# Optimization experiments

Measured on AMD Instinct MI355X. Metric: run time of the kernel, lower is better.

## Reference

```python
import jax, jax.numpy as jnp
import numpy as np

NUM_EMBED = 1024
HEAD_SIZE = 64
B, T = 4, 4096

def setup_inputs() -> dict:
    key = jax.random.key(0)
    kx, kq, kk, kv = jax.random.split(key, 4)
    scale = NUM_EMBED ** -0.5
    return {
        "x": jax.random.normal(kx, (B, T, NUM_EMBED), dtype=jnp.float32),
        "Wq": jax.random.normal(kq, (NUM_EMBED, HEAD_SIZE), dtype=jnp.float32) * scale,
        "Wk": jax.random.normal(kk, (NUM_EMBED, HEAD_SIZE), dtype=jnp.float32) * scale,
        "Wv": jax.random.normal(kv, (NUM_EMBED, HEAD_SIZE), dtype=jnp.float32) * scale,
    }

def reference(x, Wq, Wk, Wv):
    # x: [B,T,C]; Wq/Wk/Wv: [C,H]
    q = jnp.einsum('btc,ch->bth', x, Wq)
    k = jnp.einsum('btc,ch->bth', x, Wk)
    v = jnp.einsum('btc,ch->bth', x, Wv)
    Tq = x.shape[1]
    att = jnp.einsum('bth,bsh->bts', q, k) * (k.shape[-1] ** -0.5)  # [B,T,T]
    causal = jnp.tril(jnp.ones((Tq, Tq), dtype=bool))
    att = jnp.where(causal, att, -jnp.inf)
    att = jax.nn.softmax(att, axis=-1)
    # dropout p=0 (eval mode): identity
    out = jnp.einsum('bts,bsh->bth', att, v)  # [B,T,H]
    return out
```

## Files before the change

### kernel.cpp

```cpp
#include <hip/hip_runtime.h>

#define B_ 4
#define T_ 4096
#define C_ 1024
#define H_ 64

typedef _Float16 half8  __attribute__((ext_vector_type(8)));
typedef _Float16 half4_ __attribute__((ext_vector_type(4)));
typedef float    floatx4 __attribute__((ext_vector_type(4)));

#define MFMA16(a, b, c)  __builtin_amdgcn_mfma_f32_16x16x32_f16(a, b, c, 0, 0, 0)
#define MFMA16K(a, b, c) __builtin_amdgcn_mfma_f32_16x16x16f16(a, b, c, 0, 0, 0)
#define LO4(v) __builtin_shufflevector(v, v, 0, 1, 2, 3)
#define HI4(v) __builtin_shufflevector(v, v, 4, 5, 6, 7)

__global__ __launch_bounds__(256) void pack_w_kn(
    const float* __restrict__ Wq, const float* __restrict__ Wk,
    const float* __restrict__ Wv, _Float16* __restrict__ Wt2)
{
    const int idx  = blockIdx.x * 256 + threadIdx.x;
    const int mt   = idx >> 14;
    const int j    = (idx >> 10) & 15;
    const int f    = (idx >> 9) & 1;
    const int lane = (idx >> 3) & 63;
    const int jj   = idx & 7;
    const int q = lane >> 4, c = lane & 15;
    const int k  = j * 64 + f * 32 + q * 8 + jj;
    const int hp = mt * 16 + c;
    const float* W = (hp < 64) ? Wq : (hp < 128) ? Wk : Wv;
    Wt2[idx] = (_Float16)W[k * H_ + (hp & 63)];
}

__global__ __launch_bounds__(512) void qkv_kn(
    const float* __restrict__ x, const _Float16* __restrict__ Wt2,
    _Float16* __restrict__ Qh, _Float16* __restrict__ Kpk,
    _Float16* __restrict__ Vpk)
{
    __shared__ _Float16 xs[2][32][72];
    const int tid  = threadIdx.x;
    const int lane = tid & 63, w = tid >> 6;
    const int q    = lane >> 4, c = lane & 15;
    const int nt   = w & 1;
    const int mg   = w >> 1;
    const int row0 = blockIdx.x * 32;

    const int srow = tid >> 4, scol = (tid & 15) * 4;
    const float* xg = x + (size_t)(row0 + srow) * C_ + scol;

    floatx4 acc[3];
    #pragma unroll
    for (int i = 0; i < 3; ++i) acc[i] = floatx4{0.f, 0.f, 0.f, 0.f};

    float4 g = *(const float4*)xg;

    for (int j = 0; j < 16; ++j) {
        half4_ hv;
        hv[0] = (_Float16)g.x; hv[1] = (_Float16)g.y;
        hv[2] = (_Float16)g.z; hv[3] = (_Float16)g.w;
        *(half4_*)(&xs[j & 1][srow][scol]) = hv;
        __syncthreads();
        if (j < 15) g = *(const float4*)(xg + (j + 1) * 64);

        const _Float16* xrow = &xs[j & 1][nt * 16 + c][q * 8];
        const half8 b0 = *(const half8*)xrow;
        const half8 b1 = *(const half8*)(xrow + 32);

        half8 a[6];
        #pragma unroll
        for (int i = 0; i < 3; ++i) {
            const size_t fb = ((size_t)((mg * 3 + i) * 16 + j) * 2) * 512 + lane * 8;
            a[i * 2]     = *(const half8*)(Wt2 + fb);
            a[i * 2 + 1] = *(const half8*)(Wt2 + fb + 512);
        }
        #pragma unroll
        for (int i = 0; i < 3; ++i) {
            acc[i] = MFMA16(a[i * 2],     b0, acc[i]);
            acc[i] = MFMA16(a[i * 2 + 1], b1, acc[i]);
        }
    }

    const int row = row0 + nt * 16 + c;
    const int b = row >> 12, t4 = row & (T_ - 1);
    const int kt = t4 >> 6;
    const size_t tbase = ((size_t)b * 64 + kt) * 4096;
    const int mtk = (t4 >> 4) & 3;
    const int kk  = t4 & 63;

    #pragma unroll
    for (int i = 0; i < 3; ++i) {
        const int gi = mg * 3 + i;
        if (gi < 4) {
            half4_ v;
            #pragma unroll
            for (int r = 0; r < 4; ++r) v[r] = (_Float16)acc[i][r];
            *(half4_*)(Qh + (size_t)row * H_ + gi * 16 + q * 4) = v;
        } else if (gi < 8) {
            half4_ v;
            #pragma unroll
            for (int r = 0; r < 4; ++r) v[r] = (_Float16)acc[i][r];
            const int e  = gi - 4;
            const int f  = e >> 1;
            const int qa = (e * 2 + (q >> 1)) & 3;
            *(half4_*)(Kpk + tbase + ((size_t)(mtk * 2 + f) * 64 + qa * 16 + c) * 8
                       + (q & 1) * 4) = v;
        } else {
            const int mtv = gi - 8;
            const int qa2 = (kk >> 2) & 3;
            const int h4  = (kk >> 4) & 1;
            const int f2  = kk >> 5;
            const int i2  = kk & 3;
            #pragma unroll
            for (int r = 0; r < 4; ++r) {
                const int cv = q * 4 + r;
                Vpk[tbase + ((size_t)(mtv * 2 + f2) * 64 + qa2 * 16 + cv) * 8
                    + h4 * 4 + i2] = (_Float16)acc[i][r];
            }
        }
    }
}

__global__ __launch_bounds__(512, 4) void attn_kn(
    const _Float16* __restrict__ Qh, const _Float16* __restrict__ Kpk,
    const _Float16* __restrict__ Vpk, float* __restrict__ out)
{
    __shared__ __align__(16) char smem[36864];
    const int lane = threadIdx.x & 63;
    const int w    = threadIdx.x >> 6;
    const int q    = lane >> 4, c = lane & 15;

    const int bid  = blockIdx.x;
    const int xcd  = bid & 7;
    const int slot = bid >> 3;
    const int b    = xcd >> 1;
    const int e    = xcd & 1;
    const int t32  = (slot < 32) ? (127 - (2 * slot + e))
                                 : (2 * (slot - 32) + e);

    const int row0 = t32 * 32;
    const int grow = b * T_ + row0;
    const int nk   = (t32 >> 1) + 1;

    const _Float16 qs = (_Float16)0.18033688f;
    half8 bq0[2], bq1[2];
    #pragma unroll
    for (int g = 0; g < 2; ++g) {
        const _Float16* qb = Qh + (size_t)(grow + g * 16 + c) * H_;
        bq0[g] = *(const half8*)(qb + q * 8);
        bq1[g] = *(const half8*)(qb + 32 + q * 8);
        bq0[g] *= qs; bq1[g] *= qs;
    }

    floatx4 o[4][2];
    #pragma unroll
    for (int i = 0; i < 4; ++i)
        #pragma unroll
        for (int g = 0; g < 2; ++g) o[i][g] = floatx4{0.f, 0.f, 0.f, 0.f};
    float m[2] = {-3.0e38f, -3.0e38f}, l[2] = {0.f, 0.f};

    for (int kt = w; kt < nk; kt += 8) {
        const int kb = kt * 64;
        const _Float16* Kt = Kpk + ((size_t)b * 64 + kt) * 4096;
        const _Float16* Vt = Vpk + ((size_t)b * 64 + kt) * 4096;
        half8 a0[4], a1[4];

        #pragma unroll
        for (int mt = 0; mt < 4; ++mt) {
            a0[mt] = *(const half8*)(Kt + ((size_t)(mt * 2)     * 64 + lane) * 8);
            a1[mt] = *(const half8*)(Kt + ((size_t)(mt * 2 + 1) * 64 + lane) * 8);
        }
        floatx4 s[4][2];
        #pragma unroll
        for (int mt = 0; mt < 4; ++mt)
            #pragma unroll
            for (int g = 0; g < 2; ++g) {
                floatx4 z = floatx4{0.f, 0.f, 0.f, 0.f};
                z = MFMA16(a0[mt], bq0[g], z);
                s[mt][g] = MFMA16(a1[mt], bq1[g], z);
            }
        #pragma unroll
        for (int mt = 0; mt < 4; ++mt) {
            a0[mt] = *(const half8*)(Vt + ((size_t)(mt * 2)     * 64 + lane) * 8);
            a1[mt] = *(const half8*)(Vt + ((size_t)(mt * 2 + 1) * 64 + lane) * 8);
        }

        if (kt == nk - 1) {
            #pragma unroll
            for (int mt = 0; mt < 4; ++mt)
                #pragma unroll
                for (int g = 0; g < 2; ++g)
                    #pragma unroll
                    for (int r = 0; r < 4; ++r)
                        if (kb + mt * 16 + q * 4 + r > row0 + g * 16 + c)
                            s[mt][g][r] = -3.0e38f;
        }

        half4_ ph[2][4];
        #pragma unroll
        for (int g = 0; g < 2; ++g) {
            float mx = s[0][g][0];
            #pragma unroll
            for (int mt = 0; mt < 4; ++mt)
                #pragma unroll
                for (int r = 0; r < 4; ++r) mx = fmaxf(mx, s[mt][g][r]);
            mx = fmaxf(mx, __shfl_xor(mx, 16, 64));
            mx = fmaxf(mx, __shfl_xor(mx, 32, 64));
            const float mn    = fmaxf(m[g], mx);
            const float alpha = exp2f(m[g] - mn);
            float sl = 0.f;
            #pragma unroll
            for (int mt = 0; mt < 4; ++mt)
                #pragma unroll
                for (int r = 0; r < 4; ++r) {
                    const float ev = exp2f(s[mt][g][r] - mn);
                    sl += ev;
                    ph[g][mt][r] = (_Float16)ev;
                }
            sl += __shfl_xor(sl, 16, 64);
            sl += __shfl_xor(sl, 32, 64);
            l[g] = l[g] * alpha + sl;
            m[g] = mn;
            #pragma unroll
            for (int mt = 0; mt < 4; ++mt) o[mt][g] *= alpha;
        }

        #pragma unroll
        for (int mt = 0; mt < 4; ++mt) {
            const half4_ v0 = LO4(a0[mt]);
            const half4_ v1 = HI4(a0[mt]);
            const half4_ v2 = LO4(a1[mt]);
            const half4_ v3 = HI4(a1[mt]);
            #pragma unroll
            for (int g = 0; g < 2; ++g) {
                o[mt][g] = MFMA16K(v0, ph[g][0], o[mt][g]);
                o[mt][g] = MFMA16K(v1, ph[g][1], o[mt][g]);
                o[mt][g] = MFMA16K(v2, ph[g][2], o[mt][g]);
                o[mt][g] = MFMA16K(v3, ph[g][3], o[mt][g]);
            }
        }
    }

    float* Ol = (float*)smem;
    float* Ml = (float*)(smem + 34816);
    float* Ll = (float*)(smem + 35840);
    __syncthreads();
    if (q == 0) { Ml[w * 32 + c] = m[0]; Ml[w * 32 + 16 + c] = m[1]; }
    __syncthreads();
    float M0 = Ml[c], M1 = Ml[16 + c];
    #pragma unroll
    for (int w2 = 1; w2 < 8; ++w2) {
        M0 = fmaxf(M0, Ml[w2 * 32 + c]);
        M1 = fmaxf(M1, Ml[w2 * 32 + 16 + c]);
    }
    const float alpha0 = exp2f(m[0] - M0);
    const float alpha1 = exp2f(m[1] - M1);
    if (q == 0) { Ll[w * 32 + c] = l[0] * alpha0; Ll[w * 32 + 16 + c] = l[1] * alpha1; }

    const int h0 = w * 8 + q * 2;
    #pragma unroll
    for (int gp = 0; gp < 2; ++gp) {
        const float a = gp ? alpha1 : alpha0;
        #pragma unroll
        for (int mt = 0; mt < 4; ++mt)
            #pragma unroll
            for (int r = 0; r < 4; ++r)
                Ol[w * 1088 + (mt * 16 + q * 4 + r) * 17 + c] = o[mt][gp][r] * a;
        __syncthreads();
        float L = 0.f;
        #pragma unroll
        for (int w2 = 0; w2 < 8; ++w2) L += Ll[w2 * 32 + gp * 16 + c];
        const float inv = 1.f / L;
        float ox = 0.f, oy = 0.f;
        #pragma unroll
        for (int w2 = 0; w2 < 8; ++w2) {
            ox += Ol[w2 * 1088 + h0 * 17 + c];
            oy += Ol[w2 * 1088 + (h0 + 1) * 17 + c];
        }
        float2 st; st.x = ox * inv; st.y = oy * inv;
        *(float2*)(out + (size_t)(grow + gp * 16 + c) * H_ + h0) = st;
        if (gp == 0) __syncthreads();
    }
}

extern "C" void kernel_launch(void* const* d_in, const int* in_sizes, int n_in,
                              void* d_out, int out_size, void* d_ws, size_t ws_size,
                              hipStream_t stream) {
    const float* x  = (const float*)d_in[0];
    const float* Wq = (const float*)d_in[1];
    const float* Wk = (const float*)d_in[2];
    const float* Wv = (const float*)d_in[3];
    float* out = (float*)d_out;

    _Float16* ws = (_Float16*)d_ws;
    _Float16* Wt2 = ws;
    _Float16* Qh  = ws + 196608;
    _Float16* Kpk = Qh + 1048576;
    _Float16* Vpk = Kpk + 1048576;

    hipLaunchKernelGGL(pack_w_kn, dim3(768), dim3(256), 0, stream, Wq, Wk, Wv, Wt2);
    hipLaunchKernelGGL(qkv_kn, dim3((B_ * T_) / 32), dim3(512), 0, stream,
                       x, Wt2, Qh, Kpk, Vpk);
    hipLaunchKernelGGL(attn_kn, dim3(512), dim3(512), 0, stream,
                       Qh, Kpk, Vpk, out);
}
```

Baseline: 165.5 us.

## Split attention KV range four ways with atomic work queue and combine kernel

Each 32-row query tile is now split into four KV-partition work items, handed out longest-first through a global atomic counter to 1024 persistent blocks. Partial outputs, maxima and sums go to workspace, and a new combine kernel merges them and normalizes. The goal is better load balance and occupancy across the causal triangle, in exchange for an extra launch, partial-result traffic, and atomic plus per-item barrier overhead. The occupancy hint is also raised to 8 blocks per CU.

```diff
diff --git a/kernel.cpp b/kernel.cpp
--- a/kernel.cpp
+++ b/kernel.cpp
@@ -4,6 +4,7 @@
 #define T_ 4096
 #define C_ 1024
 #define H_ 64
+#define NITEMS 2048
 
 typedef _Float16 half8  __attribute__((ext_vector_type(8)));
 typedef _Float16 half4_ __attribute__((ext_vector_type(4)));
@@ -16,8 +17,10 @@
 
 __global__ __launch_bounds__(256) void pack_w_kn(
     const float* __restrict__ Wq, const float* __restrict__ Wk,
-    const float* __restrict__ Wv, _Float16* __restrict__ Wt2)
+    const float* __restrict__ Wv, _Float16* __restrict__ Wt2,
+    int* __restrict__ qctr)
 {
+    if (blockIdx.x == 0 && threadIdx.x == 0) *qctr = 0;
     const int idx  = blockIdx.x * 256 + threadIdx.x;
     const int mt   = idx >> 14;
     const int j    = (idx >> 10) & 15;
@@ -119,166 +122,211 @@
     }
 }
 
-__global__ __launch_bounds__(512, 4) void attn_kn(
+__global__ __launch_bounds__(512, 8) void attn_kn(
     const _Float16* __restrict__ Qh, const _Float16* __restrict__ Kpk,
-    const _Float16* __restrict__ Vpk, float* __restrict__ out)
+    const _Float16* __restrict__ Vpk, float* __restrict__ Opart,
+    float* __restrict__ Mp, float* __restrict__ Lp, int* __restrict__ qctr)
 {
     __shared__ __align__(16) char smem[36864];
+    __shared__ int s_item;
     const int lane = threadIdx.x & 63;
     const int w    = threadIdx.x >> 6;
     const int q    = lane >> 4, c = lane & 15;
 
-    const int bid  = blockIdx.x;
-    const int xcd  = bid & 7;
-    const int slot = bid >> 3;
-    const int b    = xcd >> 1;
-    const int e    = xcd & 1;
-    const int t32  = (slot < 32) ? (127 - (2 * slot + e))
-                                 : (2 * (slot - 32) + e);
-
-    const int row0 = t32 * 32;
-    const int grow = b * T_ + row0;
-    const int nk   = (t32 >> 1) + 1;
-
-    const _Float16 qs = (_Float16)0.18033688f;
-    half8 bq0[2], bq1[2];
-    #pragma unroll
-    for (int g = 0; g < 2; ++g) {
-        const _Float16* qb = Qh + (size_t)(grow + g * 16 + c) * H_;
-        bq0[g] = *(const half8*)(qb + q * 8);
-        bq1[g] = *(const half8*)(qb + 32 + q * 8);
-        bq0[g] *= qs; bq1[g] *= qs;
-    }
-
-    floatx4 o[4][2];
-    #pragma unroll
-    for (int i = 0; i < 4; ++i)
-        #pragma unroll
-        for (int g = 0; g < 2; ++g) o[i][g] = floatx4{0.f, 0.f, 0.f, 0.f};
-    float m[2] = {-3.0e38f, -3.0e38f}, l[2] = {0.f, 0.f};
-
-    for (int kt = w; kt < nk; kt += 8) {
-        const int kb = kt * 64;
-        const _Float16* Kt = Kpk + ((size_t)b * 64 + kt) * 4096;
-        const _Float16* Vt = Vpk + ((size_t)b * 64 + kt) * 4096;
-        half8 a0[4], a1[4];
-
-        #pragma unroll
-        for (int mt = 0; mt < 4; ++mt) {
-            a0[mt] = *(const half8*)(Kt + ((size_t)(mt * 2)     * 64 + lane) * 8);
-            a1[mt] = *(const half8*)(Kt + ((size_t)(mt * 2 + 1) * 64 + lane) * 8);
-        }
-        floatx4 s[4][2];
-        #pragma unroll
-        for (int mt = 0; mt < 4; ++mt)
-            #pragma unroll
-            for (int g = 0; g < 2; ++g) {
-                floatx4 z = floatx4{0.f, 0.f, 0.f, 0.f};
-                z = MFMA16(a0[mt], bq0[g], z);
-                s[mt][g] = MFMA16(a1[mt], bq1[g], z);
-            }
-        #pragma unroll
-        for (int mt = 0; mt < 4; ++mt) {
-            a0[mt] = *(const half8*)(Vt + ((size_t)(mt * 2)     * 64 + lane) * 8);
-            a1[mt] = *(const half8*)(Vt + ((size_t)(mt * 2 + 1) * 64 + lane) * 8);
-        }
-
-        if (kt == nk - 1) {
-            #pragma unroll
-            for (int mt = 0; mt < 4; ++mt)
-                #pragma unroll
-                for (int g = 0; g < 2; ++g)
-                    #pragma unroll
-                    for (int r = 0; r < 4; ++r)
-                        if (kb + mt * 16 + q * 4 + r > row0 + g * 16 + c)
-                            s[mt][g][r] = -3.0e38f;
-        }
-
-        half4_ ph[2][4];
-        #pragma unroll
-        for (int g = 0; g < 2; ++g) {
-            float mx = s[0][g][0];
-            #pragma unroll
-            for (int mt = 0; mt < 4; ++mt)
-                #pragma unroll
-                for (int r = 0; r < 4; ++r) mx = fmaxf(mx, s[mt][g][r]);
-            mx = fmaxf(mx, __shfl_xor(mx, 16, 64));
-            mx = fmaxf(mx, __shfl_xor(mx, 32, 64));
-            const float mn    = fmaxf(m[g], mx);
-            const float alpha = exp2f(m[g] - mn);
-            float sl = 0.f;
-            #pragma unroll
-            for (int mt = 0; mt < 4; ++mt)
-                #pragma unroll
-                for (int r = 0; r < 4; ++r) {
-                    const float ev = exp2f(s[mt][g][r] - mn);
-                    sl += ev;
-                    ph[g][mt][r] = (_Float16)ev;
-                }
-            sl += __shfl_xor(sl, 16, 64);
-            sl += __shfl_xor(sl, 32, 64);
-            l[g] = l[g] * alpha + sl;
-            m[g] = mn;
-            #pragma unroll
-            for (int mt = 0; mt < 4; ++mt) o[mt][g] *= alpha;
-        }
-
-        #pragma unroll
-        for (int mt = 0; mt < 4; ++mt) {
-            const half4_ v0 = LO4(a0[mt]);
-            const half4_ v1 = HI4(a0[mt]);
-            const half4_ v2 = LO4(a1[mt]);
-            const half4_ v3 = HI4(a1[mt]);
-            #pragma unroll
-            for (int g = 0; g < 2; ++g) {
-                o[mt][g] = MFMA16K(v0, ph[g][0], o[mt][g]);
-                o[mt][g] = MFMA16K(v1, ph[g][1], o[mt][g]);
-                o[mt][g] = MFMA16K(v2, ph[g][2], o[mt][g]);
-                o[mt][g] = MFMA16K(v3, ph[g][3], o[mt][g]);
-            }
-        }
-    }
-
     float* Ol = (float*)smem;
     float* Ml = (float*)(smem + 34816);
     float* Ll = (float*)(smem + 35840);
-    __syncthreads();
-    if (q == 0) { Ml[w * 32 + c] = m[0]; Ml[w * 32 + 16 + c] = m[1]; }
-    __syncthreads();
-    float M0 = Ml[c], M1 = Ml[16 + c];
+
+    for (;;) {
+        if (threadIdx.x == 0) s_item = atomicAdd(qctr, 1);
+        __syncthreads();
+        const int item = s_item;
+        if (item >= NITEMS) break;
+
+        const int t32     = 127 - (item >> 4);
+        const int b       = (item >> 2) & 3;
+        const int quarter = item & 3;
+        const int row0 = t32 * 32;
+        const int grow = b * T_ + row0;
+        const int nk   = (t32 >> 1) + 1;
+
+        const _Float16 qs = (_Float16)0.18033688f;
+        half8 bq0[2], bq1[2];
+        #pragma unroll
+        for (int g = 0; g < 2; ++g) {
+            const _Float16* qb = Qh + (size_t)(grow + g * 16 + c) * H_;
+            bq0[g] = *(const half8*)(qb + q * 8);
+            bq1[g] = *(const half8*)(qb + 32 + q * 8);
+            bq0[g] *= qs; bq1[g] *= qs;
+        }
+
+        floatx4 o[4][2];
+        #pragma unroll
+        for (int i = 0; i < 4; ++i)
+            #pragma unroll
+            for (int g = 0; g < 2; ++g) o[i][g] = floatx4{0.f, 0.f, 0.f, 0.f};
+        float m[2] = {-3.0e38f, -3.0e38f}, l[2] = {0.f, 0.f};
+
+        for (int kt = quarter + 4 * w; kt < nk; kt += 32) {
+            const int kb = kt * 64;
+            const _Float16* Kt = Kpk + ((size_t)b * 64 + kt) * 4096;
+            const _Float16* Vt = Vpk + ((size_t)b * 64 + kt) * 4096;
+            half8 a0[4], a1[4];
+
+            #pragma unroll
+            for (int mt = 0; mt < 4; ++mt) {
+                a0[mt] = *(const half8*)(Kt + ((size_t)(mt * 2)     * 64 + lane) * 8);
+                a1[mt] = *(const half8*)(Kt + ((size_t)(mt * 2 + 1) * 64 + lane) * 8);
+            }
+            floatx4 s[4][2];
+            #pragma unroll
+            for (int mt = 0; mt < 4; ++mt)
+                #pragma unroll
+                for (int g = 0; g < 2; ++g) {
+                    floatx4 z = floatx4{0.f, 0.f, 0.f, 0.f};
+                    z = MFMA16(a0[mt], bq0[g], z);
+                    s[mt][g] = MFMA16(a1[mt], bq1[g], z);
+                }
+            #pragma unroll
+            for (int mt = 0; mt < 4; ++mt) {
+                a0[mt] = *(const half8*)(Vt + ((size_t)(mt * 2)     * 64 + lane) * 8);
+                a1[mt] = *(const half8*)(Vt + ((size_t)(mt * 2 + 1) * 64 + lane) * 8);
+            }
+
+            if (kt == nk - 1) {
+                #pragma unroll
+                for (int mt = 0; mt < 4; ++mt)
+                    #pragma unroll
+                    for (int g = 0; g < 2; ++g)
+                        #pragma unroll
+                        for (int r = 0; r < 4; ++r)
+                            if (kb + mt * 16 + q * 4 + r > row0 + g * 16 + c)
+                                s[mt][g][r] = -3.0e38f;
+            }
+
+            half4_ ph[2][4];
+            #pragma unroll
+            for (int g = 0; g < 2; ++g) {
+                float mx = s[0][g][0];
+                #pragma unroll
+                for (int mt = 0; mt < 4; ++mt)
+                    #pragma unroll
+                    for (int r = 0; r < 4; ++r) mx = fmaxf(mx, s[mt][g][r]);
+                mx = fmaxf(mx, __shfl_xor(mx, 16, 64));
+                mx = fmaxf(mx, __shfl_xor(mx, 32, 64));
+                const float mn    = fmaxf(m[g], mx);
+                const float alpha = exp2f(m[g] - mn);
+                float sl = 0.f;
+                #pragma unroll
+                for (int mt = 0; mt < 4; ++mt)
+                    #pragma unroll
+                    for (int r = 0; r < 4; ++r) {
+                        const float ev = exp2f(s[mt][g][r] - mn);
+                        sl += ev;
+                        ph[g][mt][r] = (_Float16)ev;
+                    }
+                sl += __shfl_xor(sl, 16, 64);
+                sl += __shfl_xor(sl, 32, 64);
+                l[g] = l[g] * alpha + sl;
+                m[g] = mn;
+                #pragma unroll
+                for (int mt = 0; mt < 4; ++mt) o[mt][g] *= alpha;
+            }
+
+            #pragma unroll
+            for (int mt = 0; mt < 4; ++mt) {
+                const half4_ v0 = LO4(a0[mt]);
+                const half4_ v1 = HI4(a0[mt]);
+                const half4_ v2 = LO4(a1[mt]);
+                const half4_ v3 = HI4(a1[mt]);
+                #pragma unroll
+                for (int g = 0; g < 2; ++g) {
+                    o[mt][g] = MFMA16K(v0, ph[g][0], o[mt][g]);
+                    o[mt][g] = MFMA16K(v1, ph[g][1], o[mt][g]);
+                    o[mt][g] = MFMA16K(v2, ph[g][2], o[mt][g]);
+                    o[mt][g] = MFMA16K(v3, ph[g][3], o[mt][g]);
+                }
+            }
+        }
+
+        __syncthreads();
+        if (q == 0) { Ml[w * 32 + c] = m[0]; Ml[w * 32 + 16 + c] = m[1]; }
+        __syncthreads();
+        float M0 = Ml[c], M1 = Ml[16 + c];
+        #pragma unroll
+        for (int w2 = 1; w2 < 8; ++w2) {
+            M0 = fmaxf(M0, Ml[w2 * 32 + c]);
+            M1 = fmaxf(M1, Ml[w2 * 32 + 16 + c]);
+        }
+        const float alpha0 = exp2f(m[0] - M0);
+        const float alpha1 = exp2f(m[1] - M1);
+        if (q == 0) { Ll[w * 32 + c] = l[0] * alpha0; Ll[w * 32 + 16 + c] = l[1] * alpha1; }
+
+        const int h0 = w * 8 + q * 2;
+        float* Obase = Opart + (size_t)item * 2048;
+        #pragma unroll
+        for (int gp = 0; gp < 2; ++gp) {
+            const float a = gp ? alpha1 : alpha0;
+            #pragma unroll
+            for (int mt = 0; mt < 4; ++mt)
+                #pragma unroll
+                for (int r = 0; r < 4; ++r)
+                    Ol[w * 1088 + (mt * 16 + q * 4 + r) * 17 + c] = o[mt][gp][r] * a;
+            __syncthreads();
+            float L = 0.f;
+            #pragma unroll
+            for (int w2 = 0; w2 < 8; ++w2) L += Ll[w2 * 32 + gp * 16 + c];
+            if (w == 0 && q == 0) {
+                Mp[(size_t)item * 32 + gp * 16 + c] = gp ? M1 : M0;
+                Lp[(size_t)item * 32 + gp * 16 + c] = L;
+            }
+            float ox = 0.f, oy = 0.f;
+            #pragma unroll
+            for (int w2 = 0; w2 < 8; ++w2) {
+                ox += Ol[w2 * 1088 + h0 * 17 + c];
+                oy += Ol[w2 * 1088 + (h0 + 1) * 17 + c];
+            }
+            float2 st; st.x = ox; st.y = oy;
+            *(float2*)(Obase + (size_t)(gp * 16 + c) * 64 + h0) = st;
+            __syncthreads();
+        }
+    }
+}
+
+__global__ __launch_bounds__(256) void combine_kn(
+    const float* __restrict__ Opart, const float* __restrict__ Mp,
+    const float* __restrict__ Lp, float* __restrict__ out)
+{
+    const int cb   = blockIdx.x;
+    const int b    = cb & 3, t32 = cb >> 2;
+    const int tid  = threadIdx.x;
+    const int qrow = tid >> 3;
+    const int h0   = (tid & 7) * 8;
+    const int it0  = (127 - t32) * 16 + b * 4;
+
+    float Mv[4], Lv[4];
     #pragma unroll
-    for (int w2 = 1; w2 < 8; ++w2) {
-        M0 = fmaxf(M0, Ml[w2 * 32 + c]);
-        M1 = fmaxf(M1, Ml[w2 * 32 + 16 + c]);
-    }
-    const float alpha0 = exp2f(m[0] - M0);
-    const float alpha1 = exp2f(m[1] - M1);
-    if (q == 0) { Ll[w * 32 + c] = l[0] * alpha0; Ll[w * 32 + 16 + c] = l[1] * alpha1; }
-
-    const int h0 = w * 8 + q * 2;
+    for (int p = 0; p < 4; ++p) {
+        Mv[p] = Mp[(size_t)(it0 + p) * 32 + qrow];
+        Lv[p] = Lp[(size_t)(it0 + p) * 32 + qrow];
+    }
+    float M = fmaxf(fmaxf(Mv[0], Mv[1]), fmaxf(Mv[2], Mv[3]));
+    float L = 0.f;
+    floatx4 acc0 = floatx4{0.f, 0.f, 0.f, 0.f};
+    floatx4 acc1 = floatx4{0.f, 0.f, 0.f, 0.f};
     #pragma unroll
-    for (int gp = 0; gp < 2; ++gp) {
-        const float a = gp ? alpha1 : alpha0;
-        #pragma unroll
-        for (int mt = 0; mt < 4; ++mt)
-            #pragma unroll
-            for (int r = 0; r < 4; ++r)
-                Ol[w * 1088 + (mt * 16 + q * 4 + r) * 17 + c] = o[mt][gp][r] * a;
-        __syncthreads();
-        float L = 0.f;
-        #pragma unroll
-        for (int w2 = 0; w2 < 8; ++w2) L += Ll[w2 * 32 + gp * 16 + c];
-        const float inv = 1.f / L;
-        float ox = 0.f, oy = 0.f;
-        #pragma unroll
-        for (int w2 = 0; w2 < 8; ++w2) {
-            ox += Ol[w2 * 1088 + h0 * 17 + c];
-            oy += Ol[w2 * 1088 + (h0 + 1) * 17 + c];
-        }
-        float2 st; st.x = ox * inv; st.y = oy * inv;
-        *(float2*)(out + (size_t)(grow + gp * 16 + c) * H_ + h0) = st;
-        if (gp == 0) __syncthreads();
-    }
+    for (int p = 0; p < 4; ++p) {
+        const float a = exp2f(Mv[p] - M);
+        L += Lv[p] * a;
+        const floatx4* src = (const floatx4*)(Opart + (size_t)(it0 + p) * 2048
+                                              + (size_t)qrow * 64 + h0);
+        acc0 += src[0] * a;
+        acc1 += src[1] * a;
+    }
+    const float inv = 1.f / L;
+    floatx4* dst = (floatx4*)(out + (size_t)(b * T_ + t32 * 32 + qrow) * 64 + h0);
+    dst[0] = acc0 * inv;
+    dst[1] = acc1 * inv;
 }
 
 extern "C" void kernel_launch(void* const* d_in, const int* in_sizes, int n_in,
@@ -295,10 +343,17 @@
     _Float16* Qh  = ws + 196608;
     _Float16* Kpk = Qh + 1048576;
     _Float16* Vpk = Kpk + 1048576;
-
-    hipLaunchKernelGGL(pack_w_kn, dim3(768), dim3(256), 0, stream, Wq, Wk, Wv, Wt2);
+    float* Opart = (float*)(ws + 3342336);
+    float* Mp    = Opart + 4194304;
+    float* Lp    = Mp + 65536;
+    int*   qctr  = (int*)(Lp + 65536);
+
+    hipLaunchKernelGGL(pack_w_kn, dim3(768), dim3(256), 0, stream,
+                       Wq, Wk, Wv, Wt2, qctr);
     hipLaunchKernelGGL(qkv_kn, dim3((B_ * T_) / 32), dim3(512), 0, stream,
                        x, Wt2, Qh, Kpk, Vpk);
-    hipLaunchKernelGGL(attn_kn, dim3(512), dim3(512), 0, stream,
-                       Qh, Kpk, Vpk, out);
-}
+    hipLaunchKernelGGL(attn_kn, dim3(1024), dim3(512), 0, stream,
+                       Qh, Kpk, Vpk, Opart, Mp, Lp, qctr);
+    hipLaunchKernelGGL(combine_kn, dim3(512), dim3(256), 0, stream,
+                       Opart, Mp, Lp, out);
+}
```

New measurement: 317.6 us. 1.92x slower.
